# Kernel tuning notes

Measured on AMD Instinct MI355X. Metric: run time of the kernel, lower is better.

Reference implementation:

```python
import jax, jax.numpy as jnp
import numpy as np

B, C, H, W = 4, 192, 56, 56


def setup_inputs() -> dict:
    key = jax.random.key(0)
    k1, k2, k3 = jax.random.split(key, 3)
    x = jax.random.normal(k1, (B, C, H, W), dtype=jnp.float32)
    conv_w = jax.random.normal(k2, (C, 2 * C), dtype=jnp.float32) * (1.0 / np.sqrt(2 * C))
    conv_b = jax.random.normal(k3, (C,), dtype=jnp.float32) * 0.01
    bn_gamma = jnp.ones((C,), dtype=jnp.float32)
    bn_beta = jnp.zeros((C,), dtype=jnp.float32)
    bn_mean = jnp.zeros((C,), dtype=jnp.float32)
    bn_var = jnp.ones((C,), dtype=jnp.float32)
    return {"x": x, "conv_w": conv_w, "conv_b": conv_b, "bn_gamma": bn_gamma,
            "bn_beta": bn_beta, "bn_mean": bn_mean, "bn_var": bn_var, "K": 4}


def reference(x, conv_w, conv_b, bn_gamma, bn_beta, bn_mean, bn_var, K):
    b, c, h, w = x.shape
    shifts_h = list(range(0, h, K))          # rolls along H
    shifts_w = list(range(K, w, K))          # rolls along W
    n = len(shifts_h) + len(shifts_w)
    scale = n ** (-0.5)
    # (B, n, C, H, W): all circularly shifted copies (static shift set)
    rolled = jnp.stack([jnp.roll(x, i, axis=2) for i in shifts_h] +
                       [jnp.roll(x, j, axis=3) for j in shifts_w], axis=1)
    # scores: tanh(scale * x * x_rolled), summed over channels -> (B, n, 1, H, W)
    scores = jnp.tanh(rolled * x[:, None] * scale).sum(axis=2, keepdims=True)
    weights = jax.nn.softmax(scores, axis=1)
    out = (rolled * weights).sum(axis=1)     # (B, C, H, W)
    cat = jnp.concatenate([x, out], axis=1)  # (B, 2C, H, W)
    # 1x1 conv as GEMM over channels
    y = jnp.einsum('bchw,oc->bohw', cat, conv_w) + conv_b[None, :, None, None]
    # BatchNorm2d in eval mode (running stats)
    eps = 1e-5
    inv = bn_gamma / jnp.sqrt(bn_var + eps)
    y = (y - bn_mean[None, :, None, None]) * inv[None, :, None, None] + bn_beta[None, :, None, None]
    return jax.nn.gelu(y, approximate=False)
```

## Files before the change

kernel.cpp:

```cpp
#include <hip/hip_runtime.h>
#include <hip/hip_bf16.h>
#include <math.h>

#define BB 4
#define CC 192
#define HH 56
#define WW 56
#define HWW 3136

typedef __attribute__((ext_vector_type(8))) short short8;
typedef __attribute__((ext_vector_type(4))) float f32x4;

__device__ __forceinline__ unsigned short f2b(float f) {
    __hip_bfloat16 h = __float2bfloat16(f);
    return __builtin_bit_cast(unsigned short, h);
}
__device__ __forceinline__ float b2f(unsigned short u) {
    unsigned int x = ((unsigned int)u) << 16;
    return __builtin_bit_cast(float, x);
}
__device__ __forceinline__ void fma4(float4& a, float w, const float4& x) {
    a.x += w * x.x; a.y += w * x.y; a.z += w * x.z; a.w += w * x.w;
}

__global__ __launch_bounds__(256) void k_transpose(const float* __restrict__ x,
                                                   float* __restrict__ xt,
                                                   unsigned short* __restrict__ xth,
                                                   unsigned short* __restrict__ xtl) {
    __shared__ float tile[32][33];
    int bx = blockIdx.x, by = blockIdx.y, b = blockIdx.z;
    int tx = threadIdx.x, ty = threadIdx.y;
    int p0 = bx * 32, c0 = by * 32;
#pragma unroll
    for (int i = 0; i < 4; i++) {
        int c = c0 + ty + 8 * i;
        tile[ty + 8 * i][tx] = x[(b * CC + c) * HWW + p0 + tx];
    }
    __syncthreads();
#pragma unroll
    for (int i = 0; i < 4; i++) {
        int p = p0 + ty + 8 * i;
        float v = tile[tx][ty + 8 * i];
        size_t o = (size_t)(b * HWW + p) * CC + c0 + tx;
        xt[o] = v;
        unsigned short hi = f2b(v);
        xth[o] = hi;
        xtl[o] = f2b(v - b2f(hi));
    }
}

__global__ __launch_bounds__(256) void k_convw(const float* __restrict__ cw,
                                               unsigned short* __restrict__ cwh,
                                               unsigned short* __restrict__ cwl) {
    int i = blockIdx.x * 256 + threadIdx.x;
    if (i < CC * 576) {
        int o = i / 576, k = i % 576;
        int ks = (k >= 384) ? (k - 192) : k;
        float v = cw[o * 384 + ks];
        unsigned short hi = f2b(v);
        cwh[i] = hi;
        cwl[i] = f2b(v - b2f(hi));
    }
}

__global__ __launch_bounds__(256) void k_scores(const float* __restrict__ xt,
                                                float* __restrict__ sp) {
    __shared__ float Xs[28 * 100];
    int bid = blockIdx.x, tid = threadIdx.x;
    bool isH = bid < 896;
    int lid = isH ? bid : bid - 896;
    int half = lid & 1;
    int rp = (lid >> 1) & 1;
    int cb = lid >> 2;
    int b = cb / 56, l0 = cb % 56;
    int r0 = rp * 2;

    const float* src = xt + (size_t)(b * HWW) * CC + half * 96;
    for (int idx = tid; idx < 28 * 24; idx += 256) {
        int t2 = idx / 24, cq = idx % 24;
        int pi = (r0 + t2 / 14) + 4 * (t2 % 14);
        int pix = isH ? (pi * WW + l0) : (l0 * WW + pi);
        float4 v = *(const float4*)(src + (size_t)pix * CC + cq * 4);
        *(float4*)&Xs[t2 * 100 + cq * 4] = v;
    }
    __syncthreads();

    const float K2 = 0.38490017945975050f;
    int perCls = isH ? 105 : 91;
    int nI = 2 * perCls;
    if (tid < nI) {
        int cls = tid / perCls, p = tid % perCls;
        int a, bb;
        if (isH) {
            a = (int)((sqrtf((float)(8 * p + 1)) - 1.0f) * 0.5f);
            bb = p - (a * (a + 1)) / 2;
        } else {
            int ap = (int)((sqrtf((float)(8 * p + 1)) - 1.0f) * 0.5f);
            bb = p - (ap * (ap + 1)) / 2;
            a = ap + 1;
        }
        const float* pA = &Xs[(cls * 14 + a) * 100];
        const float* pB = &Xs[(cls * 14 + bb) * 100];
        float s0 = 0.f, s1 = 0.f, s2 = 0.f, s3 = 0.f;
#pragma unroll
        for (int q = 0; q < 24; q++) {
            float4 av = *(const float4*)(pA + q * 4);
            float4 bv = *(const float4*)(pB + q * 4);
            s0 += __builtin_amdgcn_rcpf(__expf(av.x * bv.x * K2) + 1.0f);
            s1 += __builtin_amdgcn_rcpf(__expf(av.y * bv.y * K2) + 1.0f);
            s2 += __builtin_amdgcn_rcpf(__expf(av.z * bv.z * K2) + 1.0f);
            s3 += __builtin_amdgcn_rcpf(__expf(av.w * bv.w * K2) + 1.0f);
        }
        float s = 96.0f - 2.0f * (s0 + s1 + s2 + s3);
        int r = r0 + cls;
        int sb = (half * BB + b) * 27;
        if (isH) {
            int i1 = a - bb;
            int h1 = r + 4 * a, h2 = r + 4 * bb;
            sp[(sb + i1) * HWW + h1 * WW + l0] = s;
            if (a != bb) sp[(sb + 14 - i1) * HWW + h2 * WW + l0] = s;
        } else {
            int d = a - bb;
            int w1 = r + 4 * a, w2 = r + 4 * bb;
            sp[(sb + 14 + (d - 1)) * HWW + l0 * WW + w1] = s;
            sp[(sb + 14 + (13 - d)) * HWW + l0 * WW + w2] = s;
        }
    }
}

__global__ __launch_bounds__(256) void k_acc(const float* __restrict__ xt,
                                             const float* __restrict__ sp,
                                             unsigned short* __restrict__ oHh,
                                             unsigned short* __restrict__ oHl,
                                             unsigned short* __restrict__ oWh,
                                             unsigned short* __restrict__ oWl) {
    __shared__ float Wt[14 * 56];
    int bid = blockIdx.x, tid = threadIdx.x;
    bool isH = bid < 224;
    int lid = isH ? bid : bid - 224;
    int b = lid / 56, l0 = lid % 56;

    if (tid < 56) {
        int pix = isH ? (tid * WW + l0) : (l0 * WW + tid);
        float sc[27], mx = -1e30f;
#pragma unroll
        for (int s = 0; s < 27; s++) {
            float v = sp[((0 * BB + b) * 27 + s) * HWW + pix] +
                      sp[((1 * BB + b) * 27 + s) * HWW + pix];
            sc[s] = v; mx = fmaxf(mx, v);
        }
        float sum = 0.f;
#pragma unroll
        for (int s = 0; s < 27; s++) { sc[s] = __expf(sc[s] - mx); sum += sc[s]; }
        float inv = __builtin_amdgcn_rcpf(sum);
        if (isH) {
#pragma unroll
            for (int i = 0; i < 14; i++) Wt[i * 56 + tid] = sc[i] * inv;
        } else {
#pragma unroll
            for (int j = 0; j < 13; j++) Wt[j * 56 + tid] = sc[14 + j] * inv;
        }
    }
    __syncthreads();
    if (tid < 192) {
        int r = tid & 3, q = tid >> 2;
        float4 in[14];
#pragma unroll
        for (int t = 0; t < 14; t++) {
            int pix = isH ? ((r + 4 * t) * WW + l0) : (l0 * WW + (r + 4 * t));
            in[t] = *(const float4*)(xt + (size_t)(b * HWW + pix) * CC + q * 4);
        }
        float4 acc[14] = {};
        if (isH) {
#pragma unroll
            for (int i = 0; i < 14; i++)
#pragma unroll
                for (int a = 0; a < 14; a++)
                    fma4(acc[a], Wt[i * 56 + (r + 4 * a)], in[(a - i + 14) % 14]);
        } else {
#pragma unroll
            for (int j = 0; j < 13; j++)
#pragma unroll
                for (int a = 0; a < 14; a++)
                    fma4(acc[a], Wt[j * 56 + (r + 4 * a)], in[(a - j - 1 + 14) % 14]);
        }
        unsigned short* dh = isH ? oHh : oWh;
        unsigned short* dl = isH ? oHl : oWl;
#pragma unroll
        for (int a = 0; a < 14; a++) {
            int pix = isH ? ((r + 4 * a) * WW + l0) : (l0 * WW + (r + 4 * a));
            size_t o = (size_t)(b * HWW + pix) * CC + q * 4;
            ushort4 hi4, lo4;
            hi4.x = f2b(acc[a].x); lo4.x = f2b(acc[a].x - b2f(hi4.x));
            hi4.y = f2b(acc[a].y); lo4.y = f2b(acc[a].y - b2f(hi4.y));
            hi4.z = f2b(acc[a].z); lo4.z = f2b(acc[a].z - b2f(hi4.z));
            hi4.w = f2b(acc[a].w); lo4.w = f2b(acc[a].w - b2f(hi4.w));
            *(ushort4*)(dh + o) = hi4;
            *(ushort4*)(dl + o) = lo4;
        }
    }
}

__global__ __launch_bounds__(256) void k_conv(const unsigned short* __restrict__ xth,
                                              const unsigned short* __restrict__ xtl,
                                              const unsigned short* __restrict__ oHh,
                                              const unsigned short* __restrict__ oHl,
                                              const unsigned short* __restrict__ oWh,
                                              const unsigned short* __restrict__ oWl,
                                              const unsigned short* __restrict__ cwh,
                                              const unsigned short* __restrict__ cwl,
                                              const float* __restrict__ cb,
                                              const float* __restrict__ gma,
                                              const float* __restrict__ bta,
                                              const float* __restrict__ mea,
                                              const float* __restrict__ var,
                                              float* __restrict__ y) {
    __shared__ unsigned short AB[4 * 64 * 72];
    unsigned short* Ah = AB;
    unsigned short* Al = AB + 64 * 72;
    unsigned short* Bh = AB + 2 * 64 * 72;
    unsigned short* Bl = AB + 3 * 64 * 72;
    int bm = blockIdx.x * 64, bn = blockIdx.y * 64;
    int tid = threadIdx.x, lane = tid & 63, wv = tid >> 6;

    f32x4 acc[4] = {{0,0,0,0},{0,0,0,0},{0,0,0,0},{0,0,0,0}};

    for (int kc9 = 0; kc9 < 9; kc9++) {
        const unsigned short* sh;
        const unsigned short* sl;
        int coff;
        if (kc9 < 3)      { sh = xth; sl = xtl; coff = kc9 * 64; }
        else if (kc9 < 6) { sh = oHh; sl = oHl; coff = (kc9 - 3) * 64; }
        else              { sh = oWh; sl = oWl; coff = (kc9 - 6) * 64; }
#pragma unroll
        for (int r2 = 0; r2 < 2; r2++) {
            int idx = tid + r2 * 256;
            int m = idx >> 3, kq = idx & 7;
            size_t ao = (size_t)(bm + m) * CC + coff + kq * 8;
            *(short8*)&Ah[m * 72 + kq * 8] = *(const short8*)(sh + ao);
            *(short8*)&Al[m * 72 + kq * 8] = *(const short8*)(sl + ao);
            size_t bo = (size_t)(bn + m) * 576 + kc9 * 64 + kq * 8;
            *(short8*)&Bh[m * 72 + kq * 8] = *(const short8*)(cwh + bo);
            *(short8*)&Bl[m * 72 + kq * 8] = *(const short8*)(cwl + bo);
        }
        __syncthreads();
        int n0 = wv * 16;
        int k8 = lane >> 4;
        int col = lane & 15;
#pragma unroll
        for (int ks = 0; ks < 64; ks += 32) {
            int koff = ks + k8 * 8;
            short8 bfh = *(const short8*)&Bh[(n0 + col) * 72 + koff];
            short8 bfl = *(const short8*)&Bl[(n0 + col) * 72 + koff];
#pragma unroll
            for (int fm = 0; fm < 4; fm++) {
                short8 afh = *(const short8*)&Ah[(fm * 16 + col) * 72 + koff];
                short8 afl = *(const short8*)&Al[(fm * 16 + col) * 72 + koff];
                acc[fm] = __builtin_amdgcn_mfma_f32_16x16x32_bf16(afh, bfh, acc[fm], 0, 0, 0);
                acc[fm] = __builtin_amdgcn_mfma_f32_16x16x32_bf16(afl, bfh, acc[fm], 0, 0, 0);
                acc[fm] = __builtin_amdgcn_mfma_f32_16x16x32_bf16(afh, bfl, acc[fm], 0, 0, 0);
            }
        }
        __syncthreads();
    }

    float* Ds = (float*)AB;
    {
        int col = lane & 15, rowq = lane >> 4;
#pragma unroll
        for (int fm = 0; fm < 4; fm++)
#pragma unroll
            for (int rg = 0; rg < 4; rg++)
                Ds[(fm * 16 + rowq * 4 + rg) * 68 + wv * 16 + col] = acc[fm][rg];
    }
    __syncthreads();
    {
        int o = tid >> 2, mq0 = tid & 3;
        int oo = bn + o;
        float bias = cb[oo];
        float inv  = gma[oo] * rsqrtf(var[oo] + 1e-5f);
        float mean = mea[oo], beta = bta[oo];
        int b = bm / HWW, p0 = bm % HWW;
#pragma unroll
        for (int g = 0; g < 4; g++) {
            int mq = mq0 + g * 4;
            float v[4];
#pragma unroll
            for (int j = 0; j < 4; j++) {
                float t = Ds[(mq * 4 + j) * 68 + o] + bias;
                t = (t - mean) * inv + beta;
                v[j] = 0.5f * t * (1.0f + erff(t * 0.70710678118654752f));
            }
            float4 st; st.x = v[0]; st.y = v[1]; st.z = v[2]; st.w = v[3];
            *(float4*)&y[(size_t)(b * CC + oo) * HWW + p0 + mq * 4] = st;
        }
    }
}

extern "C" void kernel_launch(void* const* d_in, const int* in_sizes, int n_in,
                              void* d_out, int out_size, void* d_ws, size_t ws_size,
                              hipStream_t stream) {
    const float* x   = (const float*)d_in[0];
    const float* cw  = (const float*)d_in[1];
    const float* cb  = (const float*)d_in[2];
    const float* gma = (const float*)d_in[3];
    const float* bta = (const float*)d_in[4];
    const float* mea = (const float*)d_in[5];
    const float* var = (const float*)d_in[6];
    float* out = (float*)d_out;

    float* ws = (float*)d_ws;
    float*          xt   = ws;
    float*          sp   = ws + 2408448;
    unsigned short* xth  = (unsigned short*)(ws + 3085824);
    unsigned short* xtl  = (unsigned short*)(ws + 4290048);
    unsigned short* oHh  = (unsigned short*)(ws + 5494272);
    unsigned short* oHl  = (unsigned short*)(ws + 6698496);
    unsigned short* oWh  = (unsigned short*)(ws + 7902720);
    unsigned short* oWl  = (unsigned short*)(ws + 9106944);
    unsigned short* cwh  = (unsigned short*)(ws + 10311168);
    unsigned short* cwl  = (unsigned short*)(ws + 10366464);

    k_transpose<<<dim3(98, 6, 4), dim3(32, 8), 0, stream>>>(x, xt, xth, xtl);
    k_convw<<<432, 256, 0, stream>>>(cw, cwh, cwl);
    k_scores<<<1792, 256, 0, stream>>>(xt, sp);
    k_acc<<<448, 256, 0, stream>>>(xt, sp, oHh, oHl, oWh, oWl);
    k_conv<<<dim3(196, 3), 256, 0, stream>>>(xth, xtl, oHh, oHl, oWh, oWl,
                                             cwh, cwl, cb, gma, bta, mea, var, out);
}
```

Measured before the change: 139.3 us.

## Merge prep kernels, split x to bf16 in GEMM, pixel-major score layout

Fuses the transpose and weight-split kernels into one launch and stops writing separate bf16 hi/lo copies of x. The GEMM now reads fp32 x and splits it into hi/lo on the fly. The score buffer becomes pixel-major with a stride of 32, so the softmax can read each pixel's scores as contiguous float4 loads. k_acc is launched with 192 threads to drop the idle warp. Together these aim to cut global memory traffic and launch overhead, at the cost of extra conversion work inside the GEMM load path.

Result: faster. 132.2 us (-5.1%).

```diff
diff --git a/kernel.cpp b/kernel.cpp
--- a/kernel.cpp
+++ b/kernel.cpp
@@ -23,43 +23,40 @@
     a.x += w * x.x; a.y += w * x.y; a.z += w * x.z; a.w += w * x.w;
 }
 
-__global__ __launch_bounds__(256) void k_transpose(const float* __restrict__ x,
-                                                   float* __restrict__ xt,
-                                                   unsigned short* __restrict__ xth,
-                                                   unsigned short* __restrict__ xtl) {
-    __shared__ float tile[32][33];
-    int bx = blockIdx.x, by = blockIdx.y, b = blockIdx.z;
-    int tx = threadIdx.x, ty = threadIdx.y;
-    int p0 = bx * 32, c0 = by * 32;
-#pragma unroll
-    for (int i = 0; i < 4; i++) {
-        int c = c0 + ty + 8 * i;
-        tile[ty + 8 * i][tx] = x[(b * CC + c) * HWW + p0 + tx];
-    }
-    __syncthreads();
-#pragma unroll
-    for (int i = 0; i < 4; i++) {
-        int p = p0 + ty + 8 * i;
-        float v = tile[tx][ty + 8 * i];
-        size_t o = (size_t)(b * HWW + p) * CC + c0 + tx;
-        xt[o] = v;
-        unsigned short hi = f2b(v);
-        xth[o] = hi;
-        xtl[o] = f2b(v - b2f(hi));
-    }
-}
-
-__global__ __launch_bounds__(256) void k_convw(const float* __restrict__ cw,
-                                               unsigned short* __restrict__ cwh,
-                                               unsigned short* __restrict__ cwl) {
-    int i = blockIdx.x * 256 + threadIdx.x;
-    if (i < CC * 576) {
-        int o = i / 576, k = i % 576;
-        int ks = (k >= 384) ? (k - 192) : k;
-        float v = cw[o * 384 + ks];
-        unsigned short hi = f2b(v);
-        cwh[i] = hi;
-        cwl[i] = f2b(v - b2f(hi));
+__global__ __launch_bounds__(256) void k_pre(const float* __restrict__ x,
+                                             float* __restrict__ xt,
+                                             const float* __restrict__ cw,
+                                             unsigned short* __restrict__ cwh,
+                                             unsigned short* __restrict__ cwl) {
+    int tid = threadIdx.x;
+    if (blockIdx.x < 2352) {
+        __shared__ float tile[32][33];
+        int id = blockIdx.x;
+        int b = id / 588, rem = id % 588;
+        int by = rem / 98, bx = rem % 98;
+        int tx = tid & 31, ty = tid >> 5;
+        int p0 = bx * 32, c0 = by * 32;
+#pragma unroll
+        for (int i = 0; i < 4; i++) {
+            int c = c0 + ty + 8 * i;
+            tile[ty + 8 * i][tx] = x[(b * CC + c) * HWW + p0 + tx];
+        }
+        __syncthreads();
+#pragma unroll
+        for (int i = 0; i < 4; i++) {
+            int p = p0 + ty + 8 * i;
+            xt[(size_t)(b * HWW + p) * CC + c0 + tx] = tile[tx][ty + 8 * i];
+        }
+    } else {
+        int i = (blockIdx.x - 2352) * 256 + tid;
+        if (i < CC * 576) {
+            int o = i / 576, k = i % 576;
+            int ks = (k >= 384) ? (k - 192) : k;
+            float v = cw[o * 384 + ks];
+            unsigned short hi = f2b(v);
+            cwh[i] = hi;
+            cwl[i] = f2b(v - b2f(hi));
+        }
     }
 }
 
@@ -113,22 +110,22 @@
         }
         float s = 96.0f - 2.0f * (s0 + s1 + s2 + s3);
         int r = r0 + cls;
-        int sb = (half * BB + b) * 27;
+        size_t base = (size_t)(half * BB + b) * HWW;
         if (isH) {
             int i1 = a - bb;
             int h1 = r + 4 * a, h2 = r + 4 * bb;
-            sp[(sb + i1) * HWW + h1 * WW + l0] = s;
-            if (a != bb) sp[(sb + 14 - i1) * HWW + h2 * WW + l0] = s;
+            sp[(base + h1 * WW + l0) * 32 + i1] = s;
+            if (a != bb) sp[(base + h2 * WW + l0) * 32 + (14 - i1)] = s;
         } else {
             int d = a - bb;
             int w1 = r + 4 * a, w2 = r + 4 * bb;
-            sp[(sb + 14 + (d - 1)) * HWW + l0 * WW + w1] = s;
-            sp[(sb + 14 + (13 - d)) * HWW + l0 * WW + w2] = s;
-        }
-    }
-}
-
-__global__ __launch_bounds__(256) void k_acc(const float* __restrict__ xt,
+            sp[(base + l0 * WW + w1) * 32 + 14 + (d - 1)] = s;
+            sp[(base + l0 * WW + w2) * 32 + 14 + (13 - d)] = s;
+        }
+    }
+}
+
+__global__ __launch_bounds__(192) void k_acc(const float* __restrict__ xt,
                                              const float* __restrict__ sp,
                                              unsigned short* __restrict__ oHh,
                                              unsigned short* __restrict__ oHl,
@@ -142,13 +139,18 @@
 
     if (tid < 56) {
         int pix = isH ? (tid * WW + l0) : (l0 * WW + tid);
-        float sc[27], mx = -1e30f;
-#pragma unroll
-        for (int s = 0; s < 27; s++) {
-            float v = sp[((0 * BB + b) * 27 + s) * HWW + pix] +
-                      sp[((1 * BB + b) * 27 + s) * HWW + pix];
-            sc[s] = v; mx = fmaxf(mx, v);
-        }
+        const float4* p0 = (const float4*)&sp[((size_t)(0 * BB + b) * HWW + pix) * 32];
+        const float4* p1 = (const float4*)&sp[((size_t)(1 * BB + b) * HWW + pix) * 32];
+        float sc[28];
+#pragma unroll
+        for (int j = 0; j < 7; j++) {
+            float4 u = p0[j], v = p1[j];
+            sc[4 * j + 0] = u.x + v.x; sc[4 * j + 1] = u.y + v.y;
+            sc[4 * j + 2] = u.z + v.z; sc[4 * j + 3] = u.w + v.w;
+        }
+        float mx = -1e30f;
+#pragma unroll
+        for (int s = 0; s < 27; s++) mx = fmaxf(mx, sc[s]);
         float sum = 0.f;
 #pragma unroll
         for (int s = 0; s < 27; s++) { sc[s] = __expf(sc[s] - mx); sum += sc[s]; }
@@ -162,7 +164,7 @@
         }
     }
     __syncthreads();
-    if (tid < 192) {
+    {
         int r = tid & 3, q = tid >> 2;
         float4 in[14];
 #pragma unroll
@@ -201,8 +203,7 @@
     }
 }
 
-__global__ __launch_bounds__(256) void k_conv(const unsigned short* __restrict__ xth,
-                                              const unsigned short* __restrict__ xtl,
+__global__ __launch_bounds__(256) void k_conv(const float* __restrict__ xt,
                                               const unsigned short* __restrict__ oHh,
                                               const unsigned short* __restrict__ oHl,
                                               const unsigned short* __restrict__ oWh,
@@ -226,19 +227,33 @@
     f32x4 acc[4] = {{0,0,0,0},{0,0,0,0},{0,0,0,0},{0,0,0,0}};
 
     for (int kc9 = 0; kc9 < 9; kc9++) {
-        const unsigned short* sh;
-        const unsigned short* sl;
-        int coff;
-        if (kc9 < 3)      { sh = xth; sl = xtl; coff = kc9 * 64; }
-        else if (kc9 < 6) { sh = oHh; sl = oHl; coff = (kc9 - 3) * 64; }
-        else              { sh = oWh; sl = oWl; coff = (kc9 - 6) * 64; }
 #pragma unroll
         for (int r2 = 0; r2 < 2; r2++) {
             int idx = tid + r2 * 256;
             int m = idx >> 3, kq = idx & 7;
-            size_t ao = (size_t)(bm + m) * CC + coff + kq * 8;
-            *(short8*)&Ah[m * 72 + kq * 8] = *(const short8*)(sh + ao);
-            *(short8*)&Al[m * 72 + kq * 8] = *(const short8*)(sl + ao);
+            if (kc9 < 3) {
+                const float* s = xt + (size_t)(bm + m) * CC + kc9 * 64 + kq * 8;
+                float4 v0 = *(const float4*)s;
+                float4 v1 = *(const float4*)(s + 4);
+                float v[8] = {v0.x, v0.y, v0.z, v0.w, v1.x, v1.y, v1.z, v1.w};
+                unsigned short hi[8], lo[8];
+#pragma unroll
+                for (int e = 0; e < 8; e++) {
+                    hi[e] = f2b(v[e]);
+                    lo[e] = f2b(v[e] - b2f(hi[e]));
+                }
+                *(short8*)&Ah[m * 72 + kq * 8] = *(short8*)hi;
+                *(short8*)&Al[m * 72 + kq * 8] = *(short8*)lo;
+            } else {
+                const unsigned short* sh;
+                const unsigned short* sl;
+                int coff;
+                if (kc9 < 6) { sh = oHh; sl = oHl; coff = (kc9 - 3) * 64; }
+                else         { sh = oWh; sl = oWl; coff = (kc9 - 6) * 64; }
+                size_t ao = (size_t)(bm + m) * CC + coff + kq * 8;
+                *(short8*)&Ah[m * 72 + kq * 8] = *(const short8*)(sh + ao);
+                *(short8*)&Al[m * 72 + kq * 8] = *(const short8*)(sl + ao);
+            }
             size_t bo = (size_t)(bn + m) * 576 + kc9 * 64 + kq * 8;
             *(short8*)&Bh[m * 72 + kq * 8] = *(const short8*)(cwh + bo);
             *(short8*)&Bl[m * 72 + kq * 8] = *(const short8*)(cwl + bo);
@@ -310,21 +325,18 @@
     float* out = (float*)d_out;
 
     float* ws = (float*)d_ws;
-    float*          xt   = ws;
-    float*          sp   = ws + 2408448;
-    unsigned short* xth  = (unsigned short*)(ws + 3085824);
-    unsigned short* xtl  = (unsigned short*)(ws + 4290048);
-    unsigned short* oHh  = (unsigned short*)(ws + 5494272);
-    unsigned short* oHl  = (unsigned short*)(ws + 6698496);
-    unsigned short* oWh  = (unsigned short*)(ws + 7902720);
-    unsigned short* oWl  = (unsigned short*)(ws + 9106944);
-    unsigned short* cwh  = (unsigned short*)(ws + 10311168);
-    unsigned short* cwl  = (unsigned short*)(ws + 10366464);
-
-    k_transpose<<<dim3(98, 6, 4), dim3(32, 8), 0, stream>>>(x, xt, xth, xtl);
-    k_convw<<<432, 256, 0, stream>>>(cw, cwh, cwl);
+    float*          xt  = ws;
+    float*          sp  = ws + 2408448;
+    unsigned short* oHh = (unsigned short*)(ws + 3211264);
+    unsigned short* oHl = (unsigned short*)(ws + 4415488);
+    unsigned short* oWh = (unsigned short*)(ws + 5619712);
+    unsigned short* oWl = (unsigned short*)(ws + 6823936);
+    unsigned short* cwh = (unsigned short*)(ws + 8028160);
+    unsigned short* cwl = (unsigned short*)(ws + 8083456);
+
+    k_pre<<<2784, 256, 0, stream>>>(x, xt, cw, cwh, cwl);
     k_scores<<<1792, 256, 0, stream>>>(xt, sp);
-    k_acc<<<448, 256, 0, stream>>>(xt, sp, oHh, oHl, oWh, oWl);
-    k_conv<<<dim3(196, 3), 256, 0, stream>>>(xth, xtl, oHh, oHl, oWh, oWl,
+    k_acc<<<448, 192, 0, stream>>>(xt, sp, oHh, oHl, oWh, oWl);
+    k_conv<<<dim3(196, 3), 256, 0, stream>>>(xt, oHh, oHl, oWh, oWl,
                                              cwh, cwl, cb, gma, bta, mea, var, out);
 }
```
